# Kernel tuning notes

Measured on AMD Instinct MI355X. Metric: run time of the kernel, lower is better.

The kernel has to match this reference:

```python
import jax, jax.numpy as jnp
import numpy as np

MARGIN = 0.2
N_CLASSES = 100
BETA_INIT = 1.2
EPS = 1e-8


def setup_inputs() -> dict:
    key = jax.random.key(0)
    k1, k2, k3 = jax.random.split(key, 3)
    BS, DIM, T = 4096, 128, 500000
    batch = jax.random.normal(k1, (BS, DIM), dtype=jnp.float32)
    labels = jax.random.randint(k2, (BS,), 0, N_CLASSES, dtype=jnp.int64)
    triplets = jax.random.randint(k3, (T, 3), 0, BS, dtype=jnp.int64)
    beta = jnp.ones((N_CLASSES,), dtype=jnp.float32) * BETA_INIT
    return {"batch": batch, "labels": labels, "triplets": triplets, "beta": beta}


def reference(batch, labels, triplets, beta):
    # Gather anchor/positive/negative embedding rows: [T, DIM]
    a = batch[triplets[:, 0]]
    p = batch[triplets[:, 1]]
    n = batch[triplets[:, 2]]
    # Euclidean distances with the module's 1e-8 stabilizer: [T]
    d_ap = jnp.sqrt(jnp.sum((a - p) ** 2, axis=-1) + EPS)
    d_an = jnp.sqrt(jnp.sum((a - n) ** 2, axis=-1) + EPS)
    # Learned per-class beta, indexed by the anchor's label: [T]
    b = beta[labels[triplets[:, 0]]]
    pos_loss = jax.nn.relu(d_ap - b + MARGIN)
    neg_loss = jax.nn.relu(b - d_an + MARGIN)
    pair_count = (jnp.sum((pos_loss > 0.0).astype(jnp.float32))
                  + jnp.sum((neg_loss > 0.0).astype(jnp.float32)))
    total = jnp.sum(pos_loss + neg_loss)
    # If no active pairs, torch code returns the (zero) unnormalized sum.
    return jnp.where(pair_count > 0.0, total / jnp.maximum(pair_count, 1.0), total)
```

## Files before the change

### kernel.cpp

```cpp
#include <hip/hip_runtime.h>

#define MARGIN 0.2f
#define EPS 1e-8f
#define GRID_BLOCKS 2048

typedef _Float16 h2 __attribute__((ext_vector_type(2)));
typedef _Float16 h8 __attribute__((ext_vector_type(8)));
union H8 { h8 v; h2 p[4]; };


__global__ __launch_bounds__(256) void convert_f32_to_f16_kernel(
    const float* __restrict__ in, _Float16* __restrict__ out, int n4)
{
    int i = blockIdx.x * blockDim.x + threadIdx.x;
    if (i < n4) {
        float4 f = *(const float4*)(in + 4 * (size_t)i);
        h2 lo, hi;
        lo.x = (_Float16)f.x; lo.y = (_Float16)f.y;
        hi.x = (_Float16)f.z; hi.y = (_Float16)f.w;
        *(h2*)(out + 4 * (size_t)i)     = lo;
        *(h2*)(out + 4 * (size_t)i + 2) = hi;
    }
}

__global__ __launch_bounds__(256) void triplet_loss_f16_kernel(
    const _Float16* __restrict__ batch16,
    const int* __restrict__ labels,
    const int* __restrict__ triplets,
    const float* __restrict__ beta,
    float* __restrict__ partial,
    int T)
{
    const int lane = threadIdx.x & 63;
    const int wid  = threadIdx.x >> 6;
    const int sub  = lane >> 2;
    const int fi   = lane & 3;

    float loss = 0.f, cnt = 0.f;

    for (int base = blockIdx.x * 64; base < T; base += gridDim.x * 64) {
        int t = base + wid * 16 + sub;
        if (t < T) {
            int ai = triplets[3 * t + 0];
            int pi = triplets[3 * t + 1];
            int ni = triplets[3 * t + 2];
            float b = beta[labels[ai]];
            const h8* __restrict__ arow = (const h8*)(batch16 + ((size_t)ai << 7));
            const h8* __restrict__ prow = (const h8*)(batch16 + ((size_t)pi << 7));
            const h8* __restrict__ nrow = (const h8*)(batch16 + ((size_t)ni << 7));
            float sap = 0.f, san = 0.f;
            #pragma unroll
            for (int k = 0; k < 4; ++k) {
                H8 a, p, n, dp, dn;
                a.v = arow[fi + 4 * k];
                p.v = prow[fi + 4 * k];
                n.v = nrow[fi + 4 * k];
                dp.v = a.v - p.v;
                dn.v = a.v - n.v;
                #pragma unroll
                for (int j = 0; j < 4; ++j) {
                    sap = __builtin_amdgcn_fdot2(dp.p[j], dp.p[j], sap, false);
                    san = __builtin_amdgcn_fdot2(dn.p[j], dn.p[j], san, false);
                }
            }
            #pragma unroll
            for (int off = 2; off >= 1; off >>= 1) {
                sap += __shfl_xor(sap, off);
                san += __shfl_xor(san, off);
            }
            float d_ap = sqrtf(sap + EPS);
            float d_an = sqrtf(san + EPS);
            float pos = fmaxf(d_ap - b + MARGIN, 0.f);
            float neg = fmaxf(b - d_an + MARGIN, 0.f);
            loss += pos + neg;
            cnt  += (pos > 0.f ? 1.f : 0.f) + (neg > 0.f ? 1.f : 0.f);
        }
    }

    #pragma unroll
    for (int off = 32; off >= 1; off >>= 1) {
        loss += __shfl_down(loss, off);
        cnt  += __shfl_down(cnt, off);
    }
    __shared__ float sl[4], sc[4];
    if (lane == 0) { sl[wid] = loss; sc[wid] = cnt; }
    __syncthreads();
    if (threadIdx.x == 0) {
        partial[blockIdx.x * 2 + 0] = sl[0] + sl[1] + sl[2] + sl[3];
        partial[blockIdx.x * 2 + 1] = sc[0] + sc[1] + sc[2] + sc[3];
    }
}


__global__ __launch_bounds__(256) void triplet_loss_f32_kernel(
    const float* __restrict__ batch,
    const int* __restrict__ labels,
    const int* __restrict__ triplets,
    const float* __restrict__ beta,
    float* __restrict__ partial,
    int T)
{
    const int lane = threadIdx.x & 63;
    const int wid  = threadIdx.x >> 6;
    const int sub  = lane >> 3;
    const int fi   = lane & 7;

    float loss = 0.f, cnt = 0.f;

    for (int base = blockIdx.x * 32; base < T; base += gridDim.x * 32) {
        int t = base + wid * 8 + sub;
        if (t < T) {
            int ai = triplets[3 * t + 0];
            int pi = triplets[3 * t + 1];
            int ni = triplets[3 * t + 2];
            float b = beta[labels[ai]];
            const float4* __restrict__ arow = (const float4*)(batch + ((size_t)ai << 7));
            const float4* __restrict__ prow = (const float4*)(batch + ((size_t)pi << 7));
            const float4* __restrict__ nrow = (const float4*)(batch + ((size_t)ni << 7));
            float sap = 0.f, san = 0.f;
            #pragma unroll
            for (int k = 0; k < 4; ++k) {
                float4 av = arow[fi + 8 * k];
                float4 pv = prow[fi + 8 * k];
                float4 nv = nrow[fi + 8 * k];
                float d;
                d = av.x - pv.x; sap += d * d;
                d = av.y - pv.y; sap += d * d;
                d = av.z - pv.z; sap += d * d;
                d = av.w - pv.w; sap += d * d;
                d = av.x - nv.x; san += d * d;
                d = av.y - nv.y; san += d * d;
                d = av.z - nv.z; san += d * d;
                d = av.w - nv.w; san += d * d;
            }
            #pragma unroll
            for (int off = 4; off >= 1; off >>= 1) {
                sap += __shfl_xor(sap, off);
                san += __shfl_xor(san, off);
            }
            float d_ap = sqrtf(sap + EPS);
            float d_an = sqrtf(san + EPS);
            float pos = fmaxf(d_ap - b + MARGIN, 0.f);
            float neg = fmaxf(b - d_an + MARGIN, 0.f);
            loss += pos + neg;
            cnt  += (pos > 0.f ? 1.f : 0.f) + (neg > 0.f ? 1.f : 0.f);
        }
    }

    #pragma unroll
    for (int off = 32; off >= 1; off >>= 1) {
        loss += __shfl_down(loss, off);
        cnt  += __shfl_down(cnt, off);
    }
    __shared__ float sl[4], sc[4];
    if (lane == 0) { sl[wid] = loss; sc[wid] = cnt; }
    __syncthreads();
    if (threadIdx.x == 0) {
        partial[blockIdx.x * 2 + 0] = sl[0] + sl[1] + sl[2] + sl[3];
        partial[blockIdx.x * 2 + 1] = sc[0] + sc[1] + sc[2] + sc[3];
    }
}


__global__ __launch_bounds__(1024) void triplet_finalize_kernel(
    const float* __restrict__ partial, float* __restrict__ out, int nblocks,
    float scale)
{
    float L = 0.f, C = 0.f;
    for (int i = threadIdx.x; i < nblocks; i += blockDim.x) {
        L += partial[2 * i + 0];
        C += partial[2 * i + 1];
    }
    #pragma unroll
    for (int off = 32; off >= 1; off >>= 1) {
        L += __shfl_down(L, off);
        C += __shfl_down(C, off);
    }
    __shared__ float sl[16], sc[16];
    int wid  = threadIdx.x >> 6;
    int lane = threadIdx.x & 63;
    int nw   = blockDim.x >> 6;
    if (lane == 0) { sl[wid] = L; sc[wid] = C; }
    __syncthreads();
    if (threadIdx.x == 0) {
        float Lt = 0.f, Ct = 0.f;
        for (int i = 0; i < nw; ++i) { Lt += sl[i]; Ct += sc[i]; }
        Lt *= scale;
        Ct *= scale;
        out[0] = (Ct > 0.f) ? (Lt / fmaxf(Ct, 1.f)) : Lt;
    }
}

extern "C" void kernel_launch(void* const* d_in, const int* in_sizes, int n_in,
                              void* d_out, int out_size, void* d_ws, size_t ws_size,
                              hipStream_t stream) {
    const float* batch    = (const float*)d_in[0];
    const int*   labels   = (const int*)d_in[1];
    const int*   triplets = (const int*)d_in[2];
    const float* beta     = (const float*)d_in[3];
    float* out = (float*)d_out;

    int nbatch = in_sizes[0];
    int T = in_sizes[2] / 3;

    size_t f16_bytes = (size_t)nbatch * sizeof(_Float16);
    size_t need = f16_bytes + (size_t)GRID_BLOCKS * 2 * sizeof(float);

    if (ws_size >= need) {
        _Float16* batch16 = (_Float16*)d_ws;
        float* partial = (float*)((char*)d_ws + f16_bytes);

        int n4 = nbatch / 4;
        convert_f32_to_f16_kernel<<<(n4 + 255) / 256, 256, 0, stream>>>(batch, batch16, n4);

        int grid = GRID_BLOCKS;
        int groups = (T + 63) / 64;
        if (grid > groups) grid = groups;
        triplet_loss_f16_kernel<<<grid, 256, 0, stream>>>(batch16, labels, triplets, beta, partial, T);
        triplet_finalize_kernel<<<1, 1024, 0, stream>>>(partial, out, grid, 0.25f);
    } else {
        float* partial = (float*)d_ws;
        int grid = GRID_BLOCKS;
        int groups = (T + 31) / 32;
        if (grid > groups) grid = groups;
        triplet_loss_f32_kernel<<<grid, 256, 0, stream>>>(batch, labels, triplets, beta, partial, T);
        triplet_finalize_kernel<<<1, 1024, 0, stream>>>(partial, out, grid, 0.125f);
    }
}
```

Baseline: 30.97 us.

## Precompute packed triplet offsets and beta in prep kernel, process two triplets per lane group

The f32-to-f16 conversion kernel now also precomputes, for each triplet, the scaled row offsets and the anchor's beta into one int4 array. The main kernel therefore does a single 16-byte load per triplet instead of three index loads plus a dependent labels-then-beta lookup. Each 8-lane group now handles two triplets per iteration, with all row loads issued up front to expose more memory-level parallelism, and out-of-range triplets are clamped and masked instead of branched around. The cost is an extra write and re-read of an 8 MB prep buffer plus more work in the prep kernel. The finalize scale changes to match the new lane layout.

New measurement: 32.61 us. +5.3%, slower.

```diff
diff --git a/kernel.cpp b/kernel.cpp
--- a/kernel.cpp
+++ b/kernel.cpp
@@ -9,72 +9,129 @@
 union H8 { h8 v; h2 p[4]; };
 
 
-__global__ __launch_bounds__(256) void convert_f32_to_f16_kernel(
-    const float* __restrict__ in, _Float16* __restrict__ out, int n4)
+__global__ __launch_bounds__(256) void prep_kernel(
+    const float* __restrict__ batch,
+    const int* __restrict__ labels,
+    const int* __restrict__ triplets,
+    const float* __restrict__ beta,
+    _Float16* __restrict__ batch16,
+    int4* __restrict__ prep,
+    int n4, int T)
 {
     int i = blockIdx.x * blockDim.x + threadIdx.x;
     if (i < n4) {
-        float4 f = *(const float4*)(in + 4 * (size_t)i);
+        float4 f = *(const float4*)(batch + 4 * (size_t)i);
         h2 lo, hi;
         lo.x = (_Float16)f.x; lo.y = (_Float16)f.y;
         hi.x = (_Float16)f.z; hi.y = (_Float16)f.w;
-        *(h2*)(out + 4 * (size_t)i)     = lo;
-        *(h2*)(out + 4 * (size_t)i + 2) = hi;
-    }
-}
-
-__global__ __launch_bounds__(256) void triplet_loss_f16_kernel(
+        *(h2*)(batch16 + 4 * (size_t)i)     = lo;
+        *(h2*)(batch16 + 4 * (size_t)i + 2) = hi;
+    }
+    if (i < T) {
+        int a = triplets[3 * i + 0];
+        int p = triplets[3 * i + 1];
+        int n = triplets[3 * i + 2];
+        float b = beta[labels[a]];
+        int4 s;
+        s.x = a << 7;
+        s.y = p << 7;
+        s.z = n << 7;
+        s.w = __float_as_int(b);
+        prep[i] = s;
+    }
+}
+
+__global__ __launch_bounds__(256) void triplet_main_kernel(
     const _Float16* __restrict__ batch16,
-    const int* __restrict__ labels,
-    const int* __restrict__ triplets,
-    const float* __restrict__ beta,
+    const int4* __restrict__ prep,
     float* __restrict__ partial,
     int T)
 {
     const int lane = threadIdx.x & 63;
     const int wid  = threadIdx.x >> 6;
-    const int sub  = lane >> 2;
-    const int fi   = lane & 3;
+    const int sub  = lane >> 3;
+    const int fi   = lane & 7;
 
     float loss = 0.f, cnt = 0.f;
+    const int Tm1 = T - 1;
 
     for (int base = blockIdx.x * 64; base < T; base += gridDim.x * 64) {
-        int t = base + wid * 16 + sub;
-        if (t < T) {
-            int ai = triplets[3 * t + 0];
-            int pi = triplets[3 * t + 1];
-            int ni = triplets[3 * t + 2];
-            float b = beta[labels[ai]];
-            const h8* __restrict__ arow = (const h8*)(batch16 + ((size_t)ai << 7));
-            const h8* __restrict__ prow = (const h8*)(batch16 + ((size_t)pi << 7));
-            const h8* __restrict__ nrow = (const h8*)(batch16 + ((size_t)ni << 7));
-            float sap = 0.f, san = 0.f;
-            #pragma unroll
-            for (int k = 0; k < 4; ++k) {
-                H8 a, p, n, dp, dn;
-                a.v = arow[fi + 4 * k];
-                p.v = prow[fi + 4 * k];
-                n.v = nrow[fi + 4 * k];
-                dp.v = a.v - p.v;
-                dn.v = a.v - n.v;
-                #pragma unroll
-                for (int j = 0; j < 4; ++j) {
-                    sap = __builtin_amdgcn_fdot2(dp.p[j], dp.p[j], sap, false);
-                    san = __builtin_amdgcn_fdot2(dn.p[j], dn.p[j], san, false);
-                }
-            }
-            #pragma unroll
-            for (int off = 2; off >= 1; off >>= 1) {
-                sap += __shfl_xor(sap, off);
-                san += __shfl_xor(san, off);
-            }
-            float d_ap = sqrtf(sap + EPS);
-            float d_an = sqrtf(san + EPS);
-            float pos = fmaxf(d_ap - b + MARGIN, 0.f);
-            float neg = fmaxf(b - d_an + MARGIN, 0.f);
-            loss += pos + neg;
-            cnt  += (pos > 0.f ? 1.f : 0.f) + (neg > 0.f ? 1.f : 0.f);
+        int tA = base + wid * 16 + sub;
+        int tB = tA + 8;
+        int cA = tA > Tm1 ? Tm1 : tA;
+        int cB = tB > Tm1 ? Tm1 : tB;
+        int4 sA = prep[cA];
+        int4 sB = prep[cB];
+
+        const h8* __restrict__ arA = (const h8*)(batch16 + (size_t)(unsigned)sA.x);
+        const h8* __restrict__ prA = (const h8*)(batch16 + (size_t)(unsigned)sA.y);
+        const h8* __restrict__ nrA = (const h8*)(batch16 + (size_t)(unsigned)sA.z);
+        const h8* __restrict__ arB = (const h8*)(batch16 + (size_t)(unsigned)sB.x);
+        const h8* __restrict__ prB = (const h8*)(batch16 + (size_t)(unsigned)sB.y);
+        const h8* __restrict__ nrB = (const h8*)(batch16 + (size_t)(unsigned)sB.z);
+
+        H8 a0A, a1A, p0A, p1A, n0A, n1A;
+        H8 a0B, a1B, p0B, p1B, n0B, n1B;
+        a0A.v = arA[fi]; a1A.v = arA[fi + 8];
+        p0A.v = prA[fi]; p1A.v = prA[fi + 8];
+        n0A.v = nrA[fi]; n1A.v = nrA[fi + 8];
+        a0B.v = arB[fi]; a1B.v = arB[fi + 8];
+        p0B.v = prB[fi]; p1B.v = prB[fi + 8];
+        n0B.v = nrB[fi]; n1B.v = nrB[fi + 8];
+
+        float sapA = 0.f, sanA = 0.f, sapB = 0.f, sanB = 0.f;
+        {
+            H8 d;
+            d.v = a0A.v - p0A.v;
+            #pragma unroll
+            for (int j = 0; j < 4; ++j) sapA = __builtin_amdgcn_fdot2(d.p[j], d.p[j], sapA, false);
+            d.v = a1A.v - p1A.v;
+            #pragma unroll
+            for (int j = 0; j < 4; ++j) sapA = __builtin_amdgcn_fdot2(d.p[j], d.p[j], sapA, false);
+            d.v = a0A.v - n0A.v;
+            #pragma unroll
+            for (int j = 0; j < 4; ++j) sanA = __builtin_amdgcn_fdot2(d.p[j], d.p[j], sanA, false);
+            d.v = a1A.v - n1A.v;
+            #pragma unroll
+            for (int j = 0; j < 4; ++j) sanA = __builtin_amdgcn_fdot2(d.p[j], d.p[j], sanA, false);
+            d.v = a0B.v - p0B.v;
+            #pragma unroll
+            for (int j = 0; j < 4; ++j) sapB = __builtin_amdgcn_fdot2(d.p[j], d.p[j], sapB, false);
+            d.v = a1B.v - p1B.v;
+            #pragma unroll
+            for (int j = 0; j < 4; ++j) sapB = __builtin_amdgcn_fdot2(d.p[j], d.p[j], sapB, false);
+            d.v = a0B.v - n0B.v;
+            #pragma unroll
+            for (int j = 0; j < 4; ++j) sanB = __builtin_amdgcn_fdot2(d.p[j], d.p[j], sanB, false);
+            d.v = a1B.v - n1B.v;
+            #pragma unroll
+            for (int j = 0; j < 4; ++j) sanB = __builtin_amdgcn_fdot2(d.p[j], d.p[j], sanB, false);
         }
+
+        #pragma unroll
+        for (int off = 4; off >= 1; off >>= 1) {
+            sapA += __shfl_xor(sapA, off);
+            sanA += __shfl_xor(sanA, off);
+            sapB += __shfl_xor(sapB, off);
+            sanB += __shfl_xor(sanB, off);
+        }
+
+        float bA = __int_as_float(sA.w);
+        float bB = __int_as_float(sB.w);
+        float mA = (tA < T) ? 1.f : 0.f;
+        float mB = (tB < T) ? 1.f : 0.f;
+
+        float dapA = sqrtf(sapA + EPS), danA = sqrtf(sanA + EPS);
+        float posA = fmaxf(dapA - bA + MARGIN, 0.f);
+        float negA = fmaxf(bA - danA + MARGIN, 0.f);
+        loss += mA * (posA + negA);
+        cnt  += mA * ((posA > 0.f ? 1.f : 0.f) + (negA > 0.f ? 1.f : 0.f));
+
+        float dapB = sqrtf(sapB + EPS), danB = sqrtf(sanB + EPS);
+        float posB = fmaxf(dapB - bB + MARGIN, 0.f);
+        float negB = fmaxf(bB - danB + MARGIN, 0.f);
+        loss += mB * (posB + negB);
+        cnt  += mB * ((posB > 0.f ? 1.f : 0.f) + (negB > 0.f ? 1.f : 0.f));
     }
 
     #pragma unroll
@@ -203,21 +260,25 @@
     int nbatch = in_sizes[0];
     int T = in_sizes[2] / 3;
 
-    size_t f16_bytes = (size_t)nbatch * sizeof(_Float16);
-    size_t need = f16_bytes + (size_t)GRID_BLOCKS * 2 * sizeof(float);
+    size_t f16_bytes  = ((size_t)nbatch * sizeof(_Float16) + 255) & ~(size_t)255;
+    size_t prep_bytes = ((size_t)T * sizeof(int4) + 255) & ~(size_t)255;
+    size_t need = f16_bytes + prep_bytes + (size_t)GRID_BLOCKS * 2 * sizeof(float);
 
     if (ws_size >= need) {
         _Float16* batch16 = (_Float16*)d_ws;
-        float* partial = (float*)((char*)d_ws + f16_bytes);
+        int4* prep        = (int4*)((char*)d_ws + f16_bytes);
+        float* partial    = (float*)((char*)d_ws + f16_bytes + prep_bytes);
 
         int n4 = nbatch / 4;
-        convert_f32_to_f16_kernel<<<(n4 + 255) / 256, 256, 0, stream>>>(batch, batch16, n4);
+        int prep_items = (T > n4) ? T : n4;
+        prep_kernel<<<(prep_items + 255) / 256, 256, 0, stream>>>(
+            batch, labels, triplets, beta, batch16, prep, n4, T);
 
         int grid = GRID_BLOCKS;
         int groups = (T + 63) / 64;
         if (grid > groups) grid = groups;
-        triplet_loss_f16_kernel<<<grid, 256, 0, stream>>>(batch16, labels, triplets, beta, partial, T);
-        triplet_finalize_kernel<<<1, 1024, 0, stream>>>(partial, out, grid, 0.25f);
+        triplet_main_kernel<<<grid, 256, 0, stream>>>(batch16, prep, partial, T);
+        triplet_finalize_kernel<<<1, 1024, 0, stream>>>(partial, out, grid, 0.125f);
     } else {
         float* partial = (float*)d_ws;
         int grid = GRID_BLOCKS;
```
